# Optimization experiments

Hardware: AMD Instinct MI355X
Metric: run time of the kernel (lower is better)

Reference implementation:

```python
import jax, jax.numpy as jnp
import numpy as np

# scipy.interpolate.splrep(x, y, s=0, k=3) on a uniform grid returns the
# interpolating cubic spline with not-a-knot boundary conditions (FITPACK
# places interior knots at x[2:-2]).  We therefore fit the not-a-knot cubic
# spline per row via a batched constant-coefficient Thomas solve and evaluate
# it at linspace(0, w-1, w*upsample_rate), matching splev(..., der=0).


def _notaknot_second_derivs(y):
    """Second derivatives M[b, i] of the not-a-knot cubic spline, uniform h=1.

    Interior eqs (i=1..w-2): M[i-1] + 4 M[i] + M[i+1] = 6*(y[i+1]-2y[i]+y[i-1])
    Not-a-knot: M[0]-2M[1]+M[2]=0 and M[w-3]-2M[w-2]+M[w-1]=0, which for a
    uniform grid decouples to M[1]=d[1]/6, M[w-2]=d[w-2]/6, leaving a plain
    [1,4,1] tridiagonal system for M[2..w-3].
    """
    B, w = y.shape
    d = 6.0 * (y[:, 2:] - 2.0 * y[:, 1:-1] + y[:, :-2])  # [B, w-2], i = 1..w-2
    M1 = d[:, 0] / 6.0    # M at index 1
    Mn2 = d[:, -1] / 6.0  # M at index w-2
    rhs = d[:, 1:-1]      # equations at i = 2..w-3, shape [B, m], m = w-4
    rhs = rhs.at[:, 0].add(-M1).at[:, -1].add(-Mn2)

    def fwd(carry, b):  # Thomas forward elimination, diag=4, off=1
        cp, dp = carry
        den = 4.0 - cp
        cp2 = 1.0 / den
        dp2 = (b - dp) / den
        return (cp2, dp2), (cp2, dp2)

    init = (jnp.zeros((), y.dtype), jnp.zeros((B,), y.dtype))
    _, (cps, dps) = jax.lax.scan(fwd, init, rhs.T)  # scan over length m

    def bwd(x_next, cd):  # back substitution
        cp, dp = cd
        x = dp - cp * x_next
        return x, x

    _, xs = jax.lax.scan(bwd, jnp.zeros((B,), y.dtype), (cps, dps), reverse=True)
    Mi = xs.T  # [B, m], M at indices 2..w-3

    # Extrapolate boundary second derivatives from the not-a-knot conditions.
    M0 = 2.0 * M1 - Mi[:, 0]
    Mw1 = 2.0 * Mn2 - Mi[:, -1]
    return jnp.concatenate(
        [M0[:, None], M1[:, None], Mi, Mn2[:, None], Mw1[:, None]], axis=1
    )  # [B, w]


def _spline_eval(y, M, upsample_rate):
    B, w = y.shape
    xq = jnp.linspace(0.0, w - 1.0, w * upsample_rate, dtype=y.dtype)  # [wq]
    i = jnp.clip(jnp.floor(xq).astype(jnp.int32), 0, w - 2)
    t = xq - i.astype(y.dtype)  # local coordinate in [0, 1]
    y0 = y[:, i]
    y1 = y[:, i + 1]
    M0 = M[:, i]
    M1 = M[:, i + 1]
    # f(t) = y0 + b t + M0/2 t^2 + (M1-M0)/6 t^3, with h=1
    b = (y1 - y0) - (2.0 * M0 + M1) / 6.0
    return y0 + t * (b + t * (0.5 * M0 + t * (M1 - M0) / 6.0))


def setup_inputs() -> dict:
    key = jax.random.key(0)
    x = jax.random.normal(key, (512, 8192), dtype=jnp.float32)
    return {"x": x, "upsample_rate": 4}


def reference(x, upsample_rate):
    M = _notaknot_second_derivs(x)
    return _spline_eval(x, M, upsample_rate)  # [B, w * upsample_rate]
```

## Files before the change

### kernel.cpp

```cpp
#include <hip/hip_runtime.h>


typedef float f32x4 __attribute__((ext_vector_type(4)));
typedef float f32x2 __attribute__((ext_vector_type(2)));

constexpr int W    = 8192;
constexpr int WU   = 32768;
constexpr int TILE = 512;
constexpr int TPB  = 4;
constexpr int HL   = 16;
constexpr int YSN  = 544;
constexpr int CN   = 516;
constexpr int KB   = 10;
constexpr int BTN  = 538;
constexpr int MTN  = 520;

constexpr float Rr  = -0.26794919243112270647f;
constexpr float W0c = -4.39230484541326386f;
constexpr float W1c =  2.78460969082652752f;
constexpr float Cg  =  0.288675134594812882f;

__global__ __launch_bounds__(256)
void spline_kernel(const float* __restrict__ x, float* __restrict__ out)
{
    const int row = blockIdx.y;
    const int t0  = blockIdx.x * TPB;
    const int tid = threadIdx.x;
    const int n   = W - 4;

    const float* __restrict__ xr   = x   + (size_t)row * W;
    float*       __restrict__ orow = out + (size_t)row * WU;

    __shared__ __align__(16) float ys[2][YSN];
    __shared__ __align__(16) f32x2 Ca[CN];
    __shared__ __align__(16) f32x2 Cb[CN];
    __shared__ float bt[BTN];
    __shared__ float Mtmp[MTN];

    auto LOAD = [&](int tile) -> f32x4 {
        f32x4 v = {0.f, 0.f, 0.f, 0.f};
        if (tid < 136) {
            int base = tile * TILE - HL + 4 * tid;
            if (tile == 0 || tile == 15) {
                #pragma unroll
                for (int e = 0; e < 4; ++e) {
                    int g = base + e;
                    g = g < 0 ? 0 : (g > W - 1 ? W - 1 : g);
                    v[e] = xr[g];
                }
            } else {
                v = *(const f32x4*)(xr + base);
            }
        }
        return v;
    };

    f32x4 regA = LOAD(t0);
    if (tid < 136) *(f32x4*)&ys[0][4 * tid] = regA;
    __syncthreads();
    regA = LOAD(t0 + 1);

    int cur = 0;
    for (int k = 0; k < TPB; ++k) {
        const int tile = t0 + k;
        const int s0   = tile * TILE;

        f32x4 regB = {0.f, 0.f, 0.f, 0.f};
        if (k + 2 < TPB) regB = LOAD(t0 + k + 2);

        float* ysc = ys[cur];
        const bool boundary = (tile == 0) || (tile == 15);

        if (!boundary) {
            if (tid < 129) {
                const f32x4* ys4 = (const f32x4*)ysc;
                float w[24];
                #pragma unroll
                for (int kk = 0; kk < 6; ++kk) {
                    f32x4 v = ys4[tid + 1 + kk];
                    w[4*kk+0]=v.x; w[4*kk+1]=v.y; w[4*kk+2]=v.z; w[4*kk+3]=v.w;
                }
                float a[5];
                #pragma unroll
                for (int d = 0; d < 5; ++d) a[d] = W0c * w[11 + d];
                float wd = W1c;
                #pragma unroll
                for (int dd = 1; dd <= 8; ++dd) {
                    #pragma unroll
                    for (int d = 0; d < 5; ++d)
                        a[d] += wd * (w[11 + d - dd] + w[11 + d + dd]);
                    wd *= Rr;
                }
                #pragma unroll
                for (int c = 0; c < 4; ++c) {
                    float y0 = w[11 + c], y1 = w[12 + c];
                    float c1 = (y1 - y0) - (2.f*a[c] + a[c+1]) * (1.f/6.f);
                    Ca[4*tid + c] = (f32x2){y0, c1};
                    Cb[4*tid + c] = (f32x2){0.5f*a[c], (a[c+1]-a[c]) * (1.f/6.f)};
                }
            }
        } else {
            const int YS0 = s0 - HL;
            auto Dp = [&](int p) -> float {
                int a2 = p - YS0;
                return 6.0f * (ysc[a2+1] - 2.0f*ysc[a2] + ysc[a2-1]);
            };
            auto M1v = [&]() -> float {
                int a2 = -YS0; return ysc[a2] - 2.f*ysc[a2+1] + ysc[a2+2];
            };
            auto Mn2v = [&]() -> float {
                int a2 = (W-1) - YS0; return ysc[a2] - 2.f*ysc[a2-1] + ysc[a2-2];
            };
            auto bval = [&](int m) -> float {
                if (m == -1 || m == n) return 0.f;
                float sgn = 1.f;
                if (m < -1)     { m = -2 - m;    sgn = -1.f; }
                else if (m > n) { m = 2*n - m;   sgn = -1.f; }
                float v = Dp(m + 2);
                if (m == 0)     v -= M1v();
                if (m == n - 1) v -= Mn2v();
                return sgn * v;
            };
            const int BT0 = s0 - 3 - KB;
            for (int idx = tid; idx < BTN; idx += 256)
                bt[idx] = bval(BT0 + idx);
            __syncthreads();
            auto convb = [&](int j) -> float {
                int base = j - 2 - BT0;
                float acc = Cg * bt[base];
                float wr  = Cg;
                #pragma unroll
                for (int d = 1; d <= KB; ++d) {
                    wr  *= Rr;
                    acc += wr * (bt[base-d] + bt[base+d]);
                }
                return acc;
            };
            for (int idx = tid; idx < 517; idx += 256) {
                int j = s0 - 1 + idx;
                j = j < 0 ? 0 : (j > W-1 ? W-1 : j);
                float m;
                if (j == 0)        m = 2.f*M1v()  - convb(2);
                else if (j == 1)   m = M1v();
                else if (j == W-2) m = Mn2v();
                else if (j == W-1) m = 2.f*Mn2v() - convb(W-3);
                else               m = convb(j);
                Mtmp[idx] = m;
            }
            __syncthreads();
            for (int idx = tid; idx < CN; idx += 256) {
                float y0 = ysc[idx + 15], y1 = ysc[idx + 16];
                float m0 = Mtmp[idx], m1 = Mtmp[idx + 1];
                Ca[idx] = (f32x2){y0, (y1 - y0) - (2.f*m0 + m1) * (1.f/6.f)};
                Cb[idx] = (f32x2){0.5f*m0, (m1 - m0) * (1.f/6.f)};
            }
        }
        __syncthreads();

        const int qbase = s0 * (WU / W);
        #pragma unroll
        for (int it = 0; it < 2; ++it) {
            int q0 = qbase + (tid + it * 256) * 4;
            unsigned num = (unsigned)q0 * 8191u;
            unsigned i0u = num / 32767u;
            int idx0 = (int)i0u - s0 + 1;
            float rr0f = (float)(num - i0u * 32767u);
            float res[4];
            #pragma unroll
            for (int u = 0; u < 4; ++u) {
                const unsigned Au = 8191u * (unsigned)u;
                const float    cu = (float)Au * (1.f/32767.f);
                bool cross = (u > 0) && (rr0f >= (float)(32767u - Au));
                int  iu = idx0 + (cross ? 1 : 0);
                float t = rr0f * (1.f/32767.f) + cu - (cross ? 1.f : 0.f);
                f32x2 ca = Ca[iu], cb = Cb[iu];
                res[u] = ca.x + t * (ca.y + t * (cb.x + t * cb.y));
            }
            *(f32x4*)(orow + q0) = (f32x4){res[0], res[1], res[2], res[3]};
        }

        if (k + 1 < TPB) {
            if (tid < 136) *(f32x4*)&ys[cur ^ 1][4 * tid] = regA;
        }
        __syncthreads();
        regA = regB;
        cur ^= 1;
    }
}

extern "C" void kernel_launch(void* const* d_in, const int* in_sizes, int n_in,
                              void* d_out, int out_size, void* d_ws, size_t ws_size,
                              hipStream_t stream) {
    const float* x = (const float*)d_in[0];
    float* out = (float*)d_out;
    const int B = in_sizes[0] / W;
    dim3 grid(W / TILE / TPB, B), block(256);
    hipLaunchKernelGGL(spline_kernel, grid, block, 0, stream, x, out);
}
```

Baseline: 24.92 us.

## Pack spline coefficients into skewed float4 LDS and simplify query indexing

Merges the two float2 coefficient arrays into a single float4 array with a skewed index to reduce LDS bank conflicts, so each lookup is one 128-bit read. The evaluation loop now reads exactly two coefficient entries per thread and uses closed-form integer arithmetic in place of the per-output division and crossing test. The next-tile staging store is moved ahead of evaluation so it overlaps the compute. The cost is that the closed-form crossing logic assumes the fixed W/upsample geometry, and the coefficient array uses slightly more padded LDS.

```diff
diff --git a/kernel.cpp b/kernel.cpp
--- a/kernel.cpp
+++ b/kernel.cpp
@@ -2,7 +2,6 @@
 
 
 typedef float f32x4 __attribute__((ext_vector_type(4)));
-typedef float f32x2 __attribute__((ext_vector_type(2)));
 
 constexpr int W    = 8192;
 constexpr int WU   = 32768;
@@ -10,7 +9,8 @@
 constexpr int TPB  = 4;
 constexpr int HL   = 16;
 constexpr int YSN  = 544;
-constexpr int CN   = 516;
+constexpr int CN   = 513;
+constexpr int CCN  = 578;
 constexpr int KB   = 10;
 constexpr int BTN  = 538;
 constexpr int MTN  = 520;
@@ -19,6 +19,8 @@
 constexpr float W0c = -4.39230484541326386f;
 constexpr float W1c =  2.78460969082652752f;
 constexpr float Cg  =  0.288675134594812882f;
+
+__device__ __forceinline__ int skew(int i) { return i + (i >> 3); }
 
 __global__ __launch_bounds__(256)
 void spline_kernel(const float* __restrict__ x, float* __restrict__ out)
@@ -32,8 +34,7 @@
     float*       __restrict__ orow = out + (size_t)row * WU;
 
     __shared__ __align__(16) float ys[2][YSN];
-    __shared__ __align__(16) f32x2 Ca[CN];
-    __shared__ __align__(16) f32x2 Cb[CN];
+    __shared__ __align__(16) f32x4 Cc[CCN];
     __shared__ float bt[BTN];
     __shared__ float Mtmp[MTN];
 
@@ -91,12 +92,17 @@
                         a[d] += wd * (w[11 + d - dd] + w[11 + d + dd]);
                     wd *= Rr;
                 }
+                const int nc = (tid == 128) ? 1 : 4;
                 #pragma unroll
                 for (int c = 0; c < 4; ++c) {
-                    float y0 = w[11 + c], y1 = w[12 + c];
-                    float c1 = (y1 - y0) - (2.f*a[c] + a[c+1]) * (1.f/6.f);
-                    Ca[4*tid + c] = (f32x2){y0, c1};
-                    Cb[4*tid + c] = (f32x2){0.5f*a[c], (a[c+1]-a[c]) * (1.f/6.f)};
+                    if (c < nc) {
+                        float y0 = w[11 + c], y1 = w[12 + c];
+                        f32x4 cc = {y0,
+                                    (y1 - y0) - (2.f*a[c] + a[c+1]) * (1.f/6.f),
+                                    0.5f * a[c],
+                                    (a[c+1] - a[c]) * (1.f/6.f)};
+                        Cc[skew(4 * tid + c)] = cc;
+                    }
                 }
             }
         } else {
@@ -136,7 +142,7 @@
                 }
                 return acc;
             };
-            for (int idx = tid; idx < 517; idx += 256) {
+            for (int idx = tid; idx < 514; idx += 256) {
                 int j = s0 - 1 + idx;
                 j = j < 0 ? 0 : (j > W-1 ? W-1 : j);
                 float m;
@@ -151,36 +157,36 @@
             for (int idx = tid; idx < CN; idx += 256) {
                 float y0 = ysc[idx + 15], y1 = ysc[idx + 16];
                 float m0 = Mtmp[idx], m1 = Mtmp[idx + 1];
-                Ca[idx] = (f32x2){y0, (y1 - y0) - (2.f*m0 + m1) * (1.f/6.f)};
-                Cb[idx] = (f32x2){0.5f*m0, (m1 - m0) * (1.f/6.f)};
+                f32x4 cc = {y0,
+                            (y1 - y0) - (2.f*m0 + m1) * (1.f/6.f),
+                            0.5f * m0,
+                            (m1 - m0) * (1.f/6.f)};
+                Cc[skew(idx)] = cc;
             }
         }
         __syncthreads();
 
-        const int qbase = s0 * (WU / W);
+        if (k + 1 < TPB) {
+            if (tid < 136) *(f32x4*)&ys[cur ^ 1][4 * tid] = regA;
+        }
+
         #pragma unroll
         for (int it = 0; it < 2; ++it) {
-            int q0 = qbase + (tid + it * 256) * 4;
-            unsigned num = (unsigned)q0 * 8191u;
-            unsigned i0u = num / 32767u;
-            int idx0 = (int)i0u - s0 + 1;
-            float rr0f = (float)(num - i0u * 32767u);
+            const int j = tid + 256 * it;
+            const int h = s0 + j;
+            const int e = 32767 - 3 * h;
+            f32x4 cA = Cc[skew(j)];
+            f32x4 cB = Cc[skew(j + 1)];
             float res[4];
             #pragma unroll
             for (int u = 0; u < 4; ++u) {
-                const unsigned Au = 8191u * (unsigned)u;
-                const float    cu = (float)Au * (1.f/32767.f);
-                bool cross = (u > 0) && (rr0f >= (float)(32767u - Au));
-                int  iu = idx0 + (cross ? 1 : 0);
-                float t = rr0f * (1.f/32767.f) + cu - (cross ? 1.f : 0.f);
-                f32x2 ca = Ca[iu], cb = Cb[iu];
-                res[u] = ca.x + t * (ca.y + t * (cb.x + t * cb.y));
-            }
-            *(f32x4*)(orow + q0) = (f32x4){res[0], res[1], res[2], res[3]};
-        }
-
-        if (k + 1 < TPB) {
-            if (tid < 136) *(f32x4*)&ys[cur ^ 1][4 * tid] = regA;
+                const int N = e + 8191 * u;
+                const bool cross = (u == 3) ? true : (N >= 32767);
+                float t = (float)(N - (cross ? 32767 : 0)) * (1.f/32767.f);
+                f32x4 cc = cross ? cB : cA;
+                res[u] = cc.x + t * (cc.y + t * (cc.z + t * cc.w));
+            }
+            *(f32x4*)(orow + 4 * h) = (f32x4){res[0], res[1], res[2], res[3]};
         }
         __syncthreads();
         regA = regB;
```

Result: faster. 24.04 us (-3.5%).
